# Kernel optimization log

Measured on AMD Instinct MI355X. Metric: run time of the kernel, lower is better.

The kernel has to match this reference:

```python
import jax, jax.numpy as jnp
import numpy as np

B, L, H, N, NL = 16, 2048, 256, 64, 4
STATE_DIM, ACTION_DIM = 32, 8
IN_DIM = STATE_DIM + ACTION_DIM
OUT_DIM = STATE_DIM + 1


def setup_inputs() -> dict:
    key = jax.random.key(0)
    ks = jax.random.split(key, 8)
    x = jax.random.normal(ks[0], (B, L, IN_DIM), jnp.float32)
    enc_w = jax.random.normal(ks[1], (H, IN_DIM), jnp.float32) / np.sqrt(IN_DIM)
    enc_b = jnp.zeros((H,), jnp.float32)
    dec_w = jax.random.normal(ks[2], (OUT_DIM, H), jnp.float32) / np.sqrt(H)
    dec_b = jnp.zeros((OUT_DIM,), jnp.float32)
    # S4D-style diagonal SSM params, per layer / per channel / per state
    lambda_re = -0.5 * jnp.ones((NL, H, N), jnp.float32)
    lambda_im = jnp.broadcast_to(np.pi * jnp.arange(N, dtype=np.float32), (NL, H, N)).astype(jnp.float32)
    c_re = jax.random.normal(ks[3], (NL, H, N), jnp.float32) * (0.5 ** 0.5)
    c_im = jax.random.normal(ks[4], (NL, H, N), jnp.float32) * (0.5 ** 0.5)
    d = jnp.ones((NL, H), jnp.float32)
    log_step = jax.random.uniform(ks[5], (NL, H), jnp.float32, np.log(1e-3), np.log(1e-1))
    ln_scale = jnp.ones((NL, H), jnp.float32)
    ln_bias = jnp.zeros((NL, H), jnp.float32)
    out_w = jax.random.normal(ks[6], (NL, H, H), jnp.float32) / np.sqrt(H)
    out_b = jnp.zeros((NL, H), jnp.float32)
    out2_w = jax.random.normal(ks[7], (NL, H, H), jnp.float32) / np.sqrt(H)
    out2_b = jnp.zeros((NL, H), jnp.float32)
    return dict(x=x, enc_w=enc_w, enc_b=enc_b, lambda_re=lambda_re, lambda_im=lambda_im,
                c_re=c_re, c_im=c_im, d=d, log_step=log_step, ln_scale=ln_scale,
                ln_bias=ln_bias, out_w=out_w, out_b=out_b, out2_w=out2_w, out2_b=out2_b,
                dec_w=dec_w, dec_b=dec_b)


def _layernorm(x, scale, bias, eps=1e-5):
    mu = jnp.mean(x, -1, keepdims=True)
    var = jnp.var(x, -1, keepdims=True)
    return (x - mu) * jax.lax.rsqrt(var + eps) * scale + bias


def _s4d_kernel(lre, lim, cre, cim, log_step):
    # lre/lim/cre/cim: (H, N); returns conv kernel (H, L)
    dt = jnp.exp(log_step)[:, None]                       # (H, 1)
    lam = (lre + 1j * lim).astype(jnp.complex64)          # (H, N)
    C = (cre + 1j * cim).astype(jnp.complex64)
    dA = jnp.exp(lam * dt)                                # ZOH discretization
    dB = (dA - 1.0) / lam                                 # (B = 1)
    t = jnp.arange(L)
    vand = jnp.exp(lam[..., None] * dt[..., None] * t)    # (H, N, L) = dA**t
    return 2.0 * jnp.real(jnp.einsum('hn,hnl->hl', C * dB, vand))


def _fft_conv(u, k):
    # u: (B, L, H), k: (H, L) -> causal long convolution via FFT
    n = 2 * L
    uf = jnp.fft.rfft(u, n=n, axis=1)                     # (B, L+1, H)
    kf = jnp.fft.rfft(k, n=n, axis=-1).T[None]            # (1, L+1, H)
    return jnp.fft.irfft(uf * kf, n=n, axis=1)[:, :L]


def reference(x, enc_w, enc_b, lambda_re, lambda_im, c_re, c_im, d, log_step,
              ln_scale, ln_bias, out_w, out_b, out2_w, out2_b, dec_w, dec_b):
    h = jnp.einsum('bli,hi->blh', x, enc_w) + enc_b
    for i in range(NL):
        skip = h
        z = _layernorm(h, ln_scale[i], ln_bias[i])
        k = _s4d_kernel(lambda_re[i], lambda_im[i], c_re[i], c_im[i], log_step[i])
        y = _fft_conv(z, k) + z * d[i]
        y = jax.nn.gelu(y)
        y = (jnp.einsum('blh,gh->blg', y, out_w[i]) + out_b[i]) * \
            jax.nn.sigmoid(jnp.einsum('blh,gh->blg', y, out2_w[i]) + out2_b[i])
        h = skip + y
    return jnp.einsum('blh,oh->blo', h, dec_w) + dec_b
```

## Files before the change

### kernel.cpp

```cpp
#include <hip/hip_runtime.h>
#include <hip/hip_bf16.h>

#define Bb 16
#define Lq 2048
#define Hh 256
#define NLay 4
#define IND 40
#define OUTD 33

typedef unsigned int uint32;
typedef unsigned short ushort_t;

typedef short bf16x8 __attribute__((ext_vector_type(8)));
typedef float f32x4 __attribute__((ext_vector_type(4)));

__device__ __forceinline__ float sigmoidf_(float x) {
    return 1.0f / (1.0f + __expf(-x));
}
__device__ __forceinline__ float gelu_(float x) {
    float x2 = x * x;
    float u = x * fmaf(0.0713548162726f, x2, 1.5957691216057308f);
    return x * sigmoidf_(u);
}
__device__ __forceinline__ unsigned short f2bf(float f) {
    uint32 u = __float_as_uint(f);
    return (unsigned short)((u + 0x7fffu + ((u >> 16) & 1u)) >> 16);
}
__device__ __forceinline__ float bf2f(unsigned short s) {
    return __uint_as_float(((uint32)s) << 16);
}
__device__ __forceinline__ void gload16(const void* g, void* l) {
    __builtin_amdgcn_global_load_lds(
        (const __attribute__((address_space(1))) unsigned int*)g,
        (__attribute__((address_space(3))) unsigned int*)l, 16, 0, 0);
}

__global__ __launch_bounds__(256) void enc_kernel(const float* __restrict__ x,
                                                  const float* __restrict__ enc_w,
                                                  const float* __restrict__ enc_b,
                                                  float* __restrict__ h) {
    __shared__ float xs[8 * IND];
    int tid = threadIdx.x;
    int t0 = blockIdx.x * 8;
    for (int i = tid; i < 8 * IND; i += 256) xs[i] = x[t0 * IND + i];
    float w[IND];
    const float4* w4 = (const float4*)(enc_w + tid * IND);
#pragma unroll
    for (int c = 0; c < 10; ++c) {
        float4 v = w4[c];
        w[4 * c] = v.x; w[4 * c + 1] = v.y; w[4 * c + 2] = v.z; w[4 * c + 3] = v.w;
    }
    float bias = enc_b[tid];
    __syncthreads();
#pragma unroll
    for (int t = 0; t < 8; ++t) {
        float acc = bias;
#pragma unroll
        for (int i = 0; i < IND; ++i) acc = fmaf(xs[t * IND + i], w[i], acc);
        h[(size_t)(t0 + t) * Hh + tid] = acc;
    }
}

__global__ __launch_bounds__(256) void wconv_kernel(const float* __restrict__ w1,
                                                    const float* __restrict__ w2,
                                                    unsigned short* __restrict__ o) {
    int idx = blockIdx.x * 256 + threadIdx.x;
    for (int i = idx; i < 65536; i += 32768) {
        float4 a = ((const float4*)w1)[i];
        ushort4 u;
        u.x = f2bf(a.x); u.y = f2bf(a.y); u.z = f2bf(a.z); u.w = f2bf(a.w);
        ((ushort4*)o)[i] = u;
        float4 b4 = ((const float4*)w2)[i];
        ushort4 v;
        v.x = f2bf(b4.x); v.y = f2bf(b4.y); v.z = f2bf(b4.z); v.w = f2bf(b4.w);
        ((ushort4*)(o + 262144))[i] = v;
    }
}

__global__ __launch_bounds__(256) void lnt_kernel(const float* __restrict__ h,
                                                  const float* __restrict__ scale,
                                                  const float* __restrict__ bias,
                                                  uint32* __restrict__ zT_u) {
    __shared__ float T[32 * 260];
    __shared__ float musab[64];
    __shared__ float scb[512];
    int tid = threadIdx.x, lane = tid & 63, wv = tid >> 6;
    size_t t0 = (size_t)blockIdx.x * 32;
    int b = (int)(t0 >> 11);
    int tloc = (int)(t0 & 2047);
    scb[tid] = scale[tid];
    scb[256 + tid] = bias[tid];
#pragma unroll
    for (int p = 0; p < 8; ++p) {
        int idx = tid + p * 256;
        int r = idx >> 6, c4 = idx & 63;
        float4 v = *(const float4*)&h[(t0 + r) * Hh + c4 * 4];
        *(float4*)&T[r * 260 + c4 * 4] = v;
    }
    __syncthreads();
    for (int tok = wv; tok < 32; tok += 4) {
        float4 v = *(const float4*)&T[tok * 260 + lane * 4];
        float s = (v.x + v.y) + (v.z + v.w);
        float q = fmaf(v.x, v.x, fmaf(v.y, v.y, fmaf(v.z, v.z, v.w * v.w)));
#pragma unroll
        for (int m = 1; m < 64; m <<= 1) {
            s += __shfl_xor(s, m, 64);
            q += __shfl_xor(q, m, 64);
        }
        if (lane == 0) {
            float mu = s * (1.0f / 256.0f);
            float var = q * (1.0f / 256.0f) - mu * mu;
            musab[tok] = mu;
            musab[32 + tok] = rsqrtf(var + 1e-5f);
        }
    }
    __syncthreads();
#pragma unroll
    for (int j = 0; j < 16; ++j) {
        int hh = wv * 64 + j * 4 + (lane >> 4);
        int tp = lane & 15;
        float v0 = T[(2 * tp) * 260 + hh];
        float v1 = T[(2 * tp + 1) * 260 + hh];
        float m0 = musab[2 * tp], r0 = musab[32 + 2 * tp];
        float m1 = musab[2 * tp + 1], r1 = musab[33 + 2 * tp];
        float sc = scb[hh], bi = scb[256 + hh];
        float o0 = fmaf((v0 - m0) * r0, sc, bi);
        float o1 = fmaf((v1 - m1) * r1, sc, bi);
        uint32 pk = ((uint32)f2bf(o1) << 16) | (uint32)f2bf(o0);
        uint32 u = (uint32)((tloc >> 1) + tp);
        uint32 usw = (u & ~28u) | ((((u >> 2) & 7u) ^ ((u >> 5) & 7u)) << 2);
        zT_u[(size_t)(b * 256 + hh) * 1024 + usw] = pk;
    }
}

__global__ __launch_bounds__(256) void k1_kernel(const float* __restrict__ lre_p,
                                                 const float* __restrict__ lim_p,
                                                 const float* __restrict__ cre_p,
                                                 const float* __restrict__ cim_p,
                                                 const float* __restrict__ d_p,
                                                 const float* __restrict__ ls_p,
                                                 unsigned short* __restrict__ tv,
                                                 unsigned short* __restrict__ eb,
                                                 float* __restrict__ da64) {
    __shared__ float pwre[65 * 65];
    __shared__ float pwim[65 * 65];
    __shared__ float GrS[64], GiS[64], ks[64];
    int il = blockIdx.x >> 8;
    int h = blockIdx.x & 255;
    lre_p += (size_t)il * 16384; lim_p += (size_t)il * 16384;
    cre_p += (size_t)il * 16384; cim_p += (size_t)il * 16384;
    d_p += il * Hh; ls_p += il * Hh;
    tv += (size_t)il * 6291456;
    eb += (size_t)il * 2097152;
    da64 += (size_t)il * 32768;
    int tid = threadIdx.x;
    int lane = tid & 63, wv = tid >> 6;

    {
        int n = lane;
        float lre = lre_p[h * 64 + n], lim = lim_p[h * 64 + n];
        float cre = cre_p[h * 64 + n], cim = cim_p[h * 64 + n];
        float dt = expf(ls_p[h]);
        float a = lre * dt, th = lim * dt;
        float s1, c1;
        sincosf(th, &s1, &c1);
        float er1 = expf(a);
        float dre = er1 * c1, dim = er1 * s1;
        if (wv == 0) {
            float dAre = dre, dAim = dim;
            float inv = 1.0f / (lre * lre + lim * lim);
            float dBre = ((dAre - 1.0f) * lre + dAim * lim) * inv;
            float dBim = (dAim * lre - (dAre - 1.0f) * lim) * inv;
            GrS[n] = cre * dBre - cim * dBim;
            GiS[n] = cre * dBim + cim * dBre;
        }
        float m0 = (float)(wv * 16);
        float sb, cb;
        sincosf(m0 * th, &sb, &cb);
        float erb = expf(m0 * a);
        float pre = erb * cb, pim = erb * sb;
#pragma unroll
        for (int mm = 0; mm < 16; ++mm) {
            int m = wv * 16 + mm;
            pwre[m * 65 + n] = pre;
            pwim[m * 65 + n] = pim;
            float nr = pre * dre - pim * dim;
            float ni = pre * dim + pim * dre;
            pre = nr; pim = ni;
        }
        if (wv == 3) {
            pwre[64 * 65 + n] = pre;
            pwim[64 * 65 + n] = pim;
            da64[h * 128 + n] = pre;
            da64[h * 128 + 64 + n] = pim;
        }
    }
    __syncthreads();

    {
        int m = tid >> 2, s = tid & 3;
        float acc = 0.0f;
#pragma unroll
        for (int i = 0; i < 16; ++i) {
            int n2 = s * 16 + i;
            acc = fmaf(GrS[n2], pwre[m * 65 + n2], fmaf(-GiS[n2], pwim[m * 65 + n2], acc));
        }
        acc += __shfl_xor(acc, 1, 64);
        acc += __shfl_xor(acc, 2, 64);
        if (s == 0) ks[m] = 2.0f * acc;
    }
    __syncthreads();

    float dh = d_p[h];
    size_t basep = (size_t)h * 24576;
#pragma unroll
    for (int i2 = 0; i2 < 16; ++i2) {
        int e = tid + i2 * 256;
        int l = e >> 6, j = e & 63;
        float v = (j < l) ? ks[l - j] : (j == l ? ks[0] + dh : 0.0f);
        int sj = (((j >> 3) ^ (l & 7)) << 3) | (j & 7);
        unsigned short hi = f2bf(v);
        tv[basep + l * 64 + sj] = hi;
        tv[basep + (64 + l) * 64 + sj] = f2bf(v - bf2f(hi));
    }
#pragma unroll
    for (int i2 = 0; i2 < 32; ++i2) {
        int e = tid + i2 * 256;
        int part = e >> 12, n = (e >> 6) & 63, j = e & 63;
        int m = 63 - j;
        float pre = pwre[m * 65 + n], pim = pwim[m * 65 + n];
        float v = part ? fmaf(GrS[n], pim, GiS[n] * pre) : fmaf(GrS[n], pre, -GiS[n] * pim);
        int sj = (((j >> 3) ^ (n & 7)) << 3) | (j & 7);
        unsigned short hi = f2bf(v);
        tv[basep + (size_t)(128 + part * 64 + n) * 64 + sj] = hi;
        tv[basep + (size_t)(256 + part * 64 + n) * 64 + sj] = f2bf(v - bf2f(hi));
    }
#pragma unroll
    for (int i2 = 0; i2 < 32; ++i2) {
        int e = tid + i2 * 256;
        int l = e >> 7, k = e & 127;
        int n = k & 63, m = l + 1;
        float v = (k < 64) ? 2.0f * pwre[m * 65 + n] : -2.0f * pwim[m * 65 + n];
        eb[(size_t)h * 8192 + l * 128 + ((((k >> 3) ^ (l & 7)) << 3) | (k & 7))] = f2bf(v);
    }
}

__global__ __launch_bounds__(256, 3) void ssm_kernel(const unsigned short* __restrict__ zT,
                                                     const unsigned short* __restrict__ tv,
                                                     const unsigned short* __restrict__ eb,
                                                     const float* __restrict__ da64,
                                                     unsigned short* __restrict__ yT) {
    static __shared__ __align__(16) char LDSA[49152];
    ushort_t* Zl = (ushort_t*)LDSA;
    ushort_t* R1 = (ushort_t*)(LDSA + 16384);
    ushort_t* R2 = (ushort_t*)(LDSA + 32768);
    ushort_t* YBl = (ushort_t*)(LDSA + 16384);
    int tid = threadIdx.x;
    int lane = tid & 63, wv = tid >> 6;
    int lr = lane & 15, lg = lane >> 4;
    int h = blockIdx.x, mb = blockIdx.y;

    float ar = da64[h * 128 + lane];
    float ai = da64[h * 128 + 64 + lane];

#pragma unroll
    for (int it = 0; it < 4; ++it) {
        int c = it * 256 + tid;
        int r = c >> 3, s = c & 7;
        int b = mb * 4 + (r >> 5), tile = r & 31;
        size_t src = ((size_t)(b * 256 + h) << 11) + tile * 64 + s * 8;
        gload16(zT + src, (char*)Zl + (it * 256 + wv * 64) * 16);
    }
#pragma unroll
    for (int it = 0; it < 4; ++it) {
        size_t src = (size_t)h * 24576 + (size_t)(it * 256 + tid) * 8;
        gload16(tv + src, (char*)R1 + (it * 256 + wv * 64) * 16);
    }
#pragma unroll
    for (int it = 0; it < 4; ++it) {
        size_t src = (size_t)h * 24576 + 8192 + (size_t)(it * 256 + tid) * 8;
        gload16(tv + src, (char*)R2 + (it * 256 + wv * 64) * 16);
    }
    __syncthreads();

    bf16x8 afz[2][2];
#pragma unroll
    for (int kk = 0; kk < 2; ++kk) {
        int row0 = wv * 32 + lr;
        int row1 = row0 + 16;
        afz[kk][0] = *(const bf16x8*)(Zl + row0 * 64 + (((kk * 4 + lg) ^ (row0 & 7)) << 3));
        afz[kk][1] = *(const bf16x8*)(Zl + row1 * 64 + (((kk * 4 + lg) ^ (row1 & 7)) << 3));
    }

    f32x4 y1[2][4], ua[2][8];
    f32x4 zf = {0.f, 0.f, 0.f, 0.f};
#pragma unroll
    for (int i = 0; i < 2; ++i) {
#pragma unroll
        for (int j = 0; j < 4; ++j) y1[i][j] = zf;
#pragma unroll
        for (int j = 0; j < 8; ++j) ua[i][j] = zf;
    }

#pragma unroll
    for (int kk = 0; kk < 2; ++kk) {
#pragma unroll
        for (int j = 0; j < 8; ++j) {
            int rw = (j < 4) ? ((j & 3) * 16 + lr) : (64 + (j & 3) * 16 + lr);
            bf16x8 bfr = *(const bf16x8*)(R1 + rw * 64 + (((kk * 4 + lg) ^ (lr & 7)) << 3));
            y1[0][j & 3] = __builtin_amdgcn_mfma_f32_16x16x32_bf16(afz[kk][0], bfr, y1[0][j & 3], 0, 0, 0);
            y1[1][j & 3] = __builtin_amdgcn_mfma_f32_16x16x32_bf16(afz[kk][1], bfr, y1[1][j & 3], 0, 0, 0);
        }
#pragma unroll
        for (int j = 0; j < 8; ++j) {
            int rw = (j < 4) ? ((j & 3) * 16 + lr) : (64 + (j & 3) * 16 + lr);
            bf16x8 bfr = *(const bf16x8*)(R2 + rw * 64 + (((kk * 4 + lg) ^ (lr & 7)) << 3));
            ua[0][j] = __builtin_amdgcn_mfma_f32_16x16x32_bf16(afz[kk][0], bfr, ua[0][j], 0, 0, 0);
            ua[1][j] = __builtin_amdgcn_mfma_f32_16x16x32_bf16(afz[kk][1], bfr, ua[1][j], 0, 0, 0);
        }
    }
    __syncthreads();

#pragma unroll
    for (int it = 0; it < 4; ++it) {
        size_t src = (size_t)h * 24576 + 16384 + (size_t)(it * 256 + tid) * 8;
        gload16(tv + src, (char*)R1 + (it * 256 + wv * 64) * 16);
    }
#pragma unroll
    for (int it = 0; it < 4; ++it) {
        size_t src = (size_t)h * 8192 + (size_t)(it * 256 + tid) * 8;
        gload16(eb + src, (char*)Zl + (it * 256 + wv * 64) * 16);
    }
    __syncthreads();

#pragma unroll
    for (int kk = 0; kk < 2; ++kk)
#pragma unroll
        for (int j = 0; j < 8; ++j) {
            int rw = (j < 4) ? ((j & 3) * 16 + lr) : (64 + (j & 3) * 16 + lr);
            bf16x8 bfr = *(const bf16x8*)(R1 + rw * 64 + (((kk * 4 + lg) ^ (lr & 7)) << 3));
            ua[0][j] = __builtin_amdgcn_mfma_f32_16x16x32_bf16(afz[kk][0], bfr, ua[0][j], 0, 0, 0);
            ua[1][j] = __builtin_amdgcn_mfma_f32_16x16x32_bf16(afz[kk][1], bfr, ua[1][j], 0, 0, 0);
        }
    __syncthreads();

    uint32* Su = (uint32*)(LDSA + 16384 + wv * 8192);
    bf16x8 afr[2][4];
    float Sre = 0.0f, Sim = 0.0f;
#pragma unroll
    for (int i = 0; i < 2; ++i) {
#pragma unroll
        for (int jj = 0; jj < 8; ++jj)
#pragma unroll
            for (int r = 0; r < 4; ++r) {
                int row = lg * 4 + r;
                int col = (jj & 3) * 16 + lr + ((jj >> 2) << 6);
                Su[row * 128 + (col ^ ((row & 7) << 2))] = __float_as_uint(ua[i][jj][r]);
            }
#pragma unroll
        for (int r = 0; r < 16; ++r) {
            int sx = (r & 7) << 2;
            int aRe = r * 128 + (lane ^ sx);
            int aIm = r * 128 + ((64 + lane) ^ sx);
            float ur = __uint_as_float(Su[aRe]);
            float ui = __uint_as_float(Su[aIm]);
            Su[aRe] = (uint32)f2bf(Sre);
            Su[aIm] = (uint32)f2bf(Sim);
            float nr = fmaf(ar, Sre, fmaf(-ai, Sim, ur));
            float ni = fmaf(ar, Sim, fmaf(ai, Sre, ui));
            Sre = nr; Sim = ni;
        }
#pragma unroll
        for (int kk = 0; kk < 4; ++kk) {
            int base = kk * 32 + lg * 8;
            int sx = (lr & 7) << 2;
            uint4 ua4 = *(const uint4*)&Su[lr * 128 + (base ^ sx)];
            uint4 ub4 = *(const uint4*)&Su[lr * 128 + ((base + 4) ^ sx)];
            uint4 pk;
            pk.x = __builtin_amdgcn_perm(ua4.y, ua4.x, 0x05040100u);
            pk.y = __builtin_amdgcn_perm(ua4.w, ua4.z, 0x05040100u);
            pk.z = __builtin_amdgcn_perm(ub4.y, ub4.x, 0x05040100u);
            pk.w = __builtin_amdgcn_perm(ub4.w, ub4.z, 0x05040100u);
            afr[i][kk] = *(bf16x8*)&pk;
        }
    }
    __syncthreads();

    f32x4 y2[2][4];
#pragma unroll
    for (int i = 0; i < 2; ++i)
#pragma unroll
        for (int j = 0; j < 4; ++j) y2[i][j] = zf;
#pragma unroll
    for (int kk = 0; kk < 4; ++kk)
#pragma unroll
        for (int j = 0; j < 4; ++j) {
            int rw = j * 16 + lr;
            bf16x8 bfr = *(const bf16x8*)(Zl + rw * 128 + (((kk * 4 + lg) ^ (rw & 7)) << 3));
            y2[0][j] = __builtin_amdgcn_mfma_f32_16x16x32_bf16(afr[0][kk], bfr, y2[0][j], 0, 0, 0);
            y2[1][j] = __builtin_amdgcn_mfma_f32_16x16x32_bf16(afr[1][kk], bfr, y2[1][j], 0, 0, 0);
        }

#pragma unroll
    for (int i = 0; i < 2; ++i)
#pragma unroll
        for (int j = 0; j < 4; ++j)
#pragma unroll
            for (int r = 0; r < 4; ++r) {
                int row = wv * 32 + i * 16 + lg * 4 + r;
                int col = j * 16 + lr;
                float y = y1[i][j][r] + y2[i][j][r];
                YBl[row * 72 + col] = f2bf(gelu_(y));
            }
    __syncthreads();

#pragma unroll
    for (int it = 0; it < 4; ++it) {
        int c = it * 256 + tid;
        int row = c >> 3, c8 = c & 7;
        int b = mb * 4 + (row >> 5), tile = row & 31;
        uint4 v = *(const uint4*)((const char*)YBl + row * 144 + c8 * 16);
        *(uint4*)(yT + (((size_t)(b * 256 + h)) << 11) + tile * 64 + c8 * 8) = v;
    }
}

__global__ __launch_bounds__(256, 2) void gated_kernel(const unsigned short* __restrict__ yT,
                                                       const unsigned short* __restrict__ w1b,
                                                       const unsigned short* __restrict__ w2b,
                                                       const float* __restrict__ b1,
                                                       const float* __restrict__ b2,
                                                       float* __restrict__ h) {
    __shared__ __align__(16) unsigned short Al[4096];
    __shared__ __align__(16) unsigned short W1l[4096];
    __shared__ __align__(16) unsigned short W2l[4096];
    int tid = threadIdx.x;
    int lane = tid & 63;
    int wv = tid >> 6;
    int wm = wv >> 1, wn = wv & 1;
    int lr = lane & 15, lg = lane >> 4;
    size_t t0 = (size_t)blockIdx.x * 128;
    int bsel = (int)(t0 >> 11);
    int tloc0 = (int)(t0 & 2047);
    int g0 = blockIdx.y * 128;

    f32x4 acc1[4][4], acc2[4][4];
    f32x4 zf = {0.f, 0.f, 0.f, 0.f};
#pragma unroll
    for (int i = 0; i < 4; ++i)
#pragma unroll
        for (int j = 0; j < 4; ++j) { acc1[i][j] = zf; acc2[i][j] = zf; }

    uint32 abase = (uint32)(size_t)(__attribute__((address_space(3))) unsigned short*)Al;

    for (int kt = 0; kt < 8; ++kt) {
        __syncthreads();
        int k0 = kt * 32;
#pragma unroll
        for (int p = 0; p < 2; ++p) {
            int s = p * 256 + tid;
            int ldsoff = (p * 256 + wv * 64) * 16;
            {
                int bi = s >> 3, w = s & 7;
                int hblk = bi >> 3, tc = bi & 7;
                int ha = hblk * 4 + (w >> 1);
                int toff = tc * 16 + (w & 1) * 8;
                gload16(yT + (((size_t)(bsel * 256 + k0 + ha)) << 11) + tloc0 + toff,
                        (char*)Al + ldsoff);
            }
            {
                int L = s >> 3, cs = s & 7;
                int cu = cs ^ (L & 7);
                int row = L * 2 + (cu >> 2), q = cu & 3;
                gload16(w1b + (size_t)(g0 + row) * 256 + k0 + q * 8, (char*)W1l + ldsoff);
                gload16(w2b + (size_t)(g0 + row) * 256 + k0 + q * 8, (char*)W2l + ldsoff);
            }
        }
        __syncthreads();
        bf16x8 a[4], f1[4], f2[4];
#pragma unroll
        for (int i = 0; i < 4; ++i) {
            int tc = wm * 4 + i;
            uint32 a0 = abase + (uint32)((lg * 2 * 8 + tc) * 128 + lr * 8);
            uint32 a1 = a0 + 1024;
            uint2 d0, d1;
            asm volatile("ds_read_b64_tr_b16 %0, %2\n\t"
                         "ds_read_b64_tr_b16 %1, %3\n\t"
                         "s_waitcnt lgkmcnt(0)"
                         : "=&v"(d0), "=&v"(d1)
                         : "v"(a0), "v"(a1));
            uint4 pk;
            pk.x = d0.x; pk.y = d0.y; pk.z = d1.x; pk.w = d1.y;
            a[i] = *(bf16x8*)&pk;
        }
#pragma unroll
        for (int j = 0; j < 4; ++j) {
            int row = wn * 64 + j * 16 + lr;
            int wadr = (row >> 1) * 64 + ((((row & 1) * 4 + lg) ^ ((row >> 1) & 7)) << 3);
            f1[j] = *(const bf16x8*)(W1l + wadr);
            f2[j] = *(const bf16x8*)(W2l + wadr);
        }
#pragma unroll
        for (int i = 0; i < 4; ++i)
#pragma unroll
            for (int j = 0; j < 4; ++j) {
                acc1[i][j] = __builtin_amdgcn_mfma_f32_16x16x32_bf16(a[i], f1[j], acc1[i][j], 0, 0, 0);
                acc2[i][j] = __builtin_amdgcn_mfma_f32_16x16x32_bf16(a[i], f2[j], acc2[i][j], 0, 0, 0);
            }
    }

    float bb1[4], bb2[4];
#pragma unroll
    for (int j = 0; j < 4; ++j) {
        int g = g0 + wn * 64 + j * 16 + lr;
        bb1[j] = b1[g];
        bb2[j] = b2[g];
    }
#pragma unroll
    for (int i = 0; i < 4; ++i)
#pragma unroll
        for (int j = 0; j < 4; ++j) {
            int g = g0 + wn * 64 + j * 16 + lr;
#pragma unroll
            for (int r = 0; r < 4; ++r) {
                size_t t = t0 + wm * 64 + i * 16 + lg * 4 + r;
                float p1 = acc1[i][j][r] + bb1[j];
                float p2 = acc2[i][j][r] + bb2[j];
                float* hp = &h[t * Hh + g];
                *hp = fmaf(p1, sigmoidf_(p2), *hp);
            }
        }
}

__global__ __launch_bounds__(256) void dec_kernel(const float* __restrict__ h,
                                                  const float* __restrict__ dec_w,
                                                  const float* __restrict__ dec_b,
                                                  float* __restrict__ out) {
    __shared__ float wT[256][36];
    __shared__ float hs[64][20];
    int tid = threadIdx.x;
    for (int idx = tid; idx < OUTD * Hh; idx += 256) {
        int o = idx >> 8, k = idx & 255;
        wT[k][o] = dec_w[idx];
    }
    size_t t0 = (size_t)blockIdx.x * 64;
    int tl = tid & 63, og = tid >> 6;
    float acc[9];
#pragma unroll
    for (int j = 0; j < 9; ++j) acc[j] = 0.0f;
    int i = tid >> 2, c = (tid & 3) * 4;
    for (int kt = 0; kt < 16; ++kt) {
        __syncthreads();
        *(float4*)&hs[i][c] = *(const float4*)&h[(t0 + i) * Hh + kt * 16 + c];
        __syncthreads();
#pragma unroll
        for (int k2 = 0; k2 < 16; ++k2) {
            float a = hs[tl][k2];
            int kk = kt * 16 + k2;
#pragma unroll
            for (int j = 0; j < 9; ++j) acc[j] = fmaf(a, wT[kk][og + 4 * j], acc[j]);
        }
    }
#pragma unroll
    for (int j = 0; j < 9; ++j) {
        int o = og + 4 * j;
        if (o < OUTD) out[(t0 + tl) * OUTD + o] = acc[j] + dec_b[o];
    }
}

extern "C" void kernel_launch(void* const* d_in, const int* in_sizes, int n_in,
                              void* d_out, int out_size, void* d_ws, size_t ws_size,
                              hipStream_t stream) {
    const float* x = (const float*)d_in[0];
    const float* enc_w = (const float*)d_in[1];
    const float* enc_b = (const float*)d_in[2];
    const float* lre = (const float*)d_in[3];
    const float* lim = (const float*)d_in[4];
    const float* cre = (const float*)d_in[5];
    const float* cim = (const float*)d_in[6];
    const float* dd = (const float*)d_in[7];
    const float* ls = (const float*)d_in[8];
    const float* lns = (const float*)d_in[9];
    const float* lnb = (const float*)d_in[10];
    const float* w1 = (const float*)d_in[11];
    const float* b1 = (const float*)d_in[12];
    const float* w2 = (const float*)d_in[13];
    const float* b2 = (const float*)d_in[14];
    const float* dw = (const float*)d_in[15];
    const float* db = (const float*)d_in[16];
    float* out = (float*)d_out;

    const size_t NTOK = (size_t)Bb * Lq;
    float* hbuf = (float*)d_ws;
    unsigned short* zT = (unsigned short*)(hbuf + NTOK * Hh);
    unsigned short* yT = zT + NTOK * Hh;
    unsigned short* wbf = yT + NTOK * Hh;
    unsigned short* tv_slab = wbf + 524288;
    unsigned short* eb_slab = tv_slab + (size_t)4 * 6291456;
    float* da64 = (float*)(eb_slab + (size_t)4 * 2097152);

    wconv_kernel<<<128, 256, 0, stream>>>(w1, w2, wbf);
    enc_kernel<<<(int)(NTOK / 8), 256, 0, stream>>>(x, enc_w, enc_b, hbuf);
    k1_kernel<<<1024, 256, 0, stream>>>(lre, lim, cre, cim, dd, ls,
                                        tv_slab, eb_slab, da64);
    for (int il = 0; il < NLay; ++il) {
        lnt_kernel<<<(int)(NTOK / 32), 256, 0, stream>>>(hbuf, lns + il * Hh, lnb + il * Hh,
                                                         (uint32*)zT);
        ssm_kernel<<<dim3(256, 4), 256, 0, stream>>>(zT,
                                                     tv_slab + (size_t)il * 6291456,
                                                     eb_slab + (size_t)il * 2097152,
                                                     da64 + (size_t)il * 32768, yT);
        gated_kernel<<<dim3(256, 2), 256, 0, stream>>>(yT,
                                                       wbf + il * 65536,
                                                       wbf + 262144 + il * 65536,
                                                       b1 + il * Hh, b2 + il * Hh, hbuf);
    }
    dec_kernel<<<(int)(NTOK / 64), 256, 0, stream>>>(hbuf, dw, db, out);
}
```

Measured before the change: 407.6 us.

## Fuse next-layer layernorm and transpose into gated GLU epilogue

The gated output kernel now handles 64 tokens across all 256 output channels per block, not 128x128 tiles, so every row of the new residual stays inside one block. Its epilogue then computes the next layer's layernorm statistics through shuffles and shared memory and writes the transposed bf16 zT directly. This removes three of the four standalone lnt_kernel launches and their extra read of h. The cost is more weight traffic per block, since each block loads both full 256x256 weight matrices, plus fewer tokens per block and extra barriers.

```diff
diff --git a/kernel.cpp b/kernel.cpp
--- a/kernel.cpp
+++ b/kernel.cpp
@@ -424,24 +424,32 @@
     }
 }
 
-__global__ __launch_bounds__(256, 2) void gated_kernel(const unsigned short* __restrict__ yT,
-                                                       const unsigned short* __restrict__ w1b,
-                                                       const unsigned short* __restrict__ w2b,
-                                                       const float* __restrict__ b1,
-                                                       const float* __restrict__ b2,
-                                                       float* __restrict__ h) {
-    __shared__ __align__(16) unsigned short Al[4096];
-    __shared__ __align__(16) unsigned short W1l[4096];
-    __shared__ __align__(16) unsigned short W2l[4096];
+__global__ __launch_bounds__(256, 2) void gatedln_kernel(const unsigned short* __restrict__ yT,
+                                                         const unsigned short* __restrict__ w1b,
+                                                         const unsigned short* __restrict__ w2b,
+                                                         const float* __restrict__ b1,
+                                                         const float* __restrict__ b2,
+                                                         float* __restrict__ h,
+                                                         const float* __restrict__ lnsc,
+                                                         const float* __restrict__ lnbi,
+                                                         uint32* __restrict__ zT_u,
+                                                         int do_ln) {
+    static __shared__ __align__(16) char GL[39424];
+    ushort_t* Al = (ushort_t*)GL;
+    ushort_t* W1l = (ushort_t*)(GL + 4096);
+    ushort_t* W2l = (ushort_t*)(GL + 20480);
+    uint32* zb = (uint32*)GL;
+    float* psum = (float*)(GL + 36864);
+    float* psq = (float*)(GL + 36864 + 1024);
+    float* musab = (float*)(GL + 38912);
+
     int tid = threadIdx.x;
     int lane = tid & 63;
     int wv = tid >> 6;
-    int wm = wv >> 1, wn = wv & 1;
     int lr = lane & 15, lg = lane >> 4;
-    size_t t0 = (size_t)blockIdx.x * 128;
+    size_t t0 = (size_t)blockIdx.x * 64;
     int bsel = (int)(t0 >> 11);
     int tloc0 = (int)(t0 & 2047);
-    int g0 = blockIdx.y * 128;
 
     f32x4 acc1[4][4], acc2[4][4];
     f32x4 zf = {0.f, 0.f, 0.f, 0.f};
@@ -455,33 +463,31 @@
     for (int kt = 0; kt < 8; ++kt) {
         __syncthreads();
         int k0 = kt * 32;
-#pragma unroll
-        for (int p = 0; p < 2; ++p) {
+        {
+            int bi = tid >> 3, w = tid & 7;
+            int hblk = bi >> 2, tc = bi & 3;
+            int ha = hblk * 4 + (w >> 1);
+            int toff = tc * 16 + (w & 1) * 8;
+            gload16(yT + (((size_t)(bsel * 256 + k0 + ha)) << 11) + tloc0 + toff,
+                    (char*)Al + (wv * 64) * 16);
+        }
+#pragma unroll
+        for (int p = 0; p < 4; ++p) {
             int s = p * 256 + tid;
             int ldsoff = (p * 256 + wv * 64) * 16;
-            {
-                int bi = s >> 3, w = s & 7;
-                int hblk = bi >> 3, tc = bi & 7;
-                int ha = hblk * 4 + (w >> 1);
-                int toff = tc * 16 + (w & 1) * 8;
-                gload16(yT + (((size_t)(bsel * 256 + k0 + ha)) << 11) + tloc0 + toff,
-                        (char*)Al + ldsoff);
-            }
-            {
-                int L = s >> 3, cs = s & 7;
-                int cu = cs ^ (L & 7);
-                int row = L * 2 + (cu >> 2), q = cu & 3;
-                gload16(w1b + (size_t)(g0 + row) * 256 + k0 + q * 8, (char*)W1l + ldsoff);
-                gload16(w2b + (size_t)(g0 + row) * 256 + k0 + q * 8, (char*)W2l + ldsoff);
-            }
+            int L = s >> 3, cs = s & 7;
+            int cu = cs ^ (L & 7);
+            int row = L * 2 + (cu >> 2), q = cu & 3;
+            gload16(w1b + (size_t)row * 256 + k0 + q * 8, (char*)W1l + ldsoff);
+            gload16(w2b + (size_t)row * 256 + k0 + q * 8, (char*)W2l + ldsoff);
         }
         __syncthreads();
         bf16x8 a[4], f1[4], f2[4];
 #pragma unroll
         for (int i = 0; i < 4; ++i) {
-            int tc = wm * 4 + i;
-            uint32 a0 = abase + (uint32)((lg * 2 * 8 + tc) * 128 + lr * 8);
-            uint32 a1 = a0 + 1024;
+            int tc = i;
+            uint32 a0 = abase + (uint32)(((lg * 2 * 4 + tc) * 128) + lr * 8);
+            uint32 a1 = a0 + 512;
             uint2 d0, d1;
             asm volatile("ds_read_b64_tr_b16 %0, %2\n\t"
                          "ds_read_b64_tr_b16 %1, %3\n\t"
@@ -494,7 +500,7 @@
         }
 #pragma unroll
         for (int j = 0; j < 4; ++j) {
-            int row = wn * 64 + j * 16 + lr;
+            int row = wv * 64 + j * 16 + lr;
             int wadr = (row >> 1) * 64 + ((((row & 1) * 4 + lg) ^ ((row >> 1) & 7)) << 3);
             f1[j] = *(const bf16x8*)(W1l + wadr);
             f2[j] = *(const bf16x8*)(W2l + wadr);
@@ -507,28 +513,80 @@
                 acc2[i][j] = __builtin_amdgcn_mfma_f32_16x16x32_bf16(a[i], f2[j], acc2[i][j], 0, 0, 0);
             }
     }
-
-    float bb1[4], bb2[4];
+    __syncthreads();
+
+    float bb1[4], bb2[4], scv[4], biv[4];
 #pragma unroll
     for (int j = 0; j < 4; ++j) {
-        int g = g0 + wn * 64 + j * 16 + lr;
+        int g = wv * 64 + j * 16 + lr;
         bb1[j] = b1[g];
         bb2[j] = b2[g];
-    }
+        if (do_ln) { scv[j] = lnsc[g]; biv[j] = lnbi[g]; }
+    }
+
 #pragma unroll
     for (int i = 0; i < 4; ++i)
 #pragma unroll
-        for (int j = 0; j < 4; ++j) {
-            int g = g0 + wn * 64 + j * 16 + lr;
-#pragma unroll
-            for (int r = 0; r < 4; ++r) {
-                size_t t = t0 + wm * 64 + i * 16 + lg * 4 + r;
+        for (int r = 0; r < 4; ++r) {
+            int row = i * 16 + lg * 4 + r;
+            size_t t = t0 + row;
+            float srow = 0.0f, qrow = 0.0f;
+#pragma unroll
+            for (int j = 0; j < 4; ++j) {
+                int g = wv * 64 + j * 16 + lr;
                 float p1 = acc1[i][j][r] + bb1[j];
                 float p2 = acc2[i][j][r] + bb2[j];
                 float* hp = &h[t * Hh + g];
-                *hp = fmaf(p1, sigmoidf_(p2), *hp);
+                float hv = fmaf(p1, sigmoidf_(p2), *hp);
+                *hp = hv;
+                acc1[i][j][r] = hv;
+                srow += hv;
+                qrow = fmaf(hv, hv, qrow);
             }
-        }
+            if (do_ln) {
+                srow += __shfl_xor(srow, 1, 64); qrow += __shfl_xor(qrow, 1, 64);
+                srow += __shfl_xor(srow, 2, 64); qrow += __shfl_xor(qrow, 2, 64);
+                srow += __shfl_xor(srow, 4, 64); qrow += __shfl_xor(qrow, 4, 64);
+                srow += __shfl_xor(srow, 8, 64); qrow += __shfl_xor(qrow, 8, 64);
+                if (lr == 0) { psum[row * 4 + wv] = srow; psq[row * 4 + wv] = qrow; }
+            }
+        }
+
+    if (do_ln) {
+        __syncthreads();
+        if (tid < 64) {
+            float s = (psum[tid * 4] + psum[tid * 4 + 1]) + (psum[tid * 4 + 2] + psum[tid * 4 + 3]);
+            float q = (psq[tid * 4] + psq[tid * 4 + 1]) + (psq[tid * 4 + 2] + psq[tid * 4 + 3]);
+            float mu = s * (1.0f / 256.0f);
+            float var = q * (1.0f / 256.0f) - mu * mu;
+            musab[tid] = mu;
+            musab[64 + tid] = rsqrtf(var + 1e-5f);
+        }
+        __syncthreads();
+#pragma unroll
+        for (int i = 0; i < 4; ++i)
+#pragma unroll
+            for (int j = 0; j < 4; ++j) {
+                int g = wv * 64 + j * 16 + lr;
+                int row0 = i * 16 + lg * 4;
+                float z0 = fmaf((acc1[i][j][0] - musab[row0]) * musab[64 + row0], scv[j], biv[j]);
+                float z1 = fmaf((acc1[i][j][1] - musab[row0 + 1]) * musab[64 + row0 + 1], scv[j], biv[j]);
+                float z2 = fmaf((acc1[i][j][2] - musab[row0 + 2]) * musab[64 + row0 + 2], scv[j], biv[j]);
+                float z3 = fmaf((acc1[i][j][3] - musab[row0 + 3]) * musab[64 + row0 + 3], scv[j], biv[j]);
+                zb[g * 36 + i * 8 + lg * 2 + 0] = ((uint32)f2bf(z1) << 16) | (uint32)f2bf(z0);
+                zb[g * 36 + i * 8 + lg * 2 + 1] = ((uint32)f2bf(z3) << 16) | (uint32)f2bf(z2);
+            }
+        __syncthreads();
+        int tile7 = (int)((t0 >> 6) & 7);
+#pragma unroll
+        for (int it = 0; it < 8; ++it) {
+            int s2 = it * 256 + tid;
+            int g2 = s2 >> 3, c = s2 & 7;
+            uint4 v = *(const uint4*)&zb[g2 * 36 + c * 4];
+            int csw = c ^ tile7;
+            *(uint4*)(zT_u + (size_t)(bsel * 256 + g2) * 1024 + (tloc0 >> 1) + csw * 4) = v;
+        }
+    }
 }
 
 __global__ __launch_bounds__(256) void dec_kernel(const float* __restrict__ h,
@@ -602,17 +660,18 @@
     enc_kernel<<<(int)(NTOK / 8), 256, 0, stream>>>(x, enc_w, enc_b, hbuf);
     k1_kernel<<<1024, 256, 0, stream>>>(lre, lim, cre, cim, dd, ls,
                                         tv_slab, eb_slab, da64);
+    lnt_kernel<<<(int)(NTOK / 32), 256, 0, stream>>>(hbuf, lns, lnb, (uint32*)zT);
     for (int il = 0; il < NLay; ++il) {
-        lnt_kernel<<<(int)(NTOK / 32), 256, 0, stream>>>(hbuf, lns + il * Hh, lnb + il * Hh,
-                                                         (uint32*)zT);
         ssm_kernel<<<dim3(256, 4), 256, 0, stream>>>(zT,
                                                      tv_slab + (size_t)il * 6291456,
                                                      eb_slab + (size_t)il * 2097152,
                                                      da64 + (size_t)il * 32768, yT);
-        gated_kernel<<<dim3(256, 2), 256, 0, stream>>>(yT,
-                                                       wbf + il * 65536,
-                                                       wbf + 262144 + il * 65536,
-                                                       b1 + il * Hh, b2 + il * Hh, hbuf);
+        int nl = (il < NLay - 1) ? (il + 1) : il;
+        gatedln_kernel<<<(int)(NTOK / 64), 256, 0, stream>>>(
+            yT, wbf + il * 65536, wbf + 262144 + il * 65536,
+            b1 + il * Hh, b2 + il * Hh, hbuf,
+            lns + nl * Hh, lnb + nl * Hh, (uint32*)zT,
+            (il < NLay - 1) ? 1 : 0);
     }
     dec_kernel<<<(int)(NTOK / 64), 256, 0, stream>>>(hbuf, dw, db, out);
 }
```

After: 409.0 us. About the same (+0.3%).
